# Optimization experiments

Hardware: AMD Instinct MI355X
Metric: run time of the kernel (lower is better)

## Reference

```python
import jax, jax.numpy as jnp
import numpy as np

B, L, DM = 4, 1024, 2048
H, KV, HD = 32, 4, 128
G = H // KV
E, TOPK, MI = 16, 8, 128
EPS = 1e-6
THETA = 1e6


def rms_norm(x, w):
    return x * jax.lax.rsqrt(jnp.mean(x * x, axis=-1, keepdims=True) + EPS) * w


def rotate_half(x):
    x1, x2 = jnp.split(x, 2, axis=-1)
    return jnp.concatenate([-x2, x1], axis=-1)


def setup_inputs() -> dict:
    key = jax.random.key(0)
    ks = jax.random.split(key, 10)
    s = 0.02
    # RoPE tables: [L, HD] broadcast to [B, L, HD]
    inv_freq = 1.0 / (THETA ** (jnp.arange(0, HD, 2, dtype=jnp.float32) / HD))
    ang = jnp.arange(L, dtype=jnp.float32)[:, None] * inv_freq[None, :]
    emb = jnp.concatenate([ang, ang], axis=-1)
    cos = jnp.broadcast_to(jnp.cos(emb)[None], (B, L, HD)).astype(jnp.float32)
    sin = jnp.broadcast_to(jnp.sin(emb)[None], (B, L, HD)).astype(jnp.float32)
    return {
        "x": jax.random.normal(ks[0], (B, L, DM), jnp.float32),
        "cos": cos,
        "sin": sin,
        "norm_attn_w": jnp.ones((DM,), jnp.float32),
        "q_w": jax.random.normal(ks[1], (H * HD, DM), jnp.float32) * s,
        "k_w": jax.random.normal(ks[2], (KV * HD, DM), jnp.float32) * s,
        "v_w": jax.random.normal(ks[3], (KV * HD, DM), jnp.float32) * s,
        "qn_w": jnp.ones((HD,), jnp.float32),
        "kn_w": jnp.ones((HD,), jnp.float32),
        "o_w": jax.random.normal(ks[4], (DM, H * HD), jnp.float32) * s,
        "norm_mlp_w": jnp.ones((DM,), jnp.float32),
        "router_w": jax.random.normal(ks[5], (E, DM), jnp.float32) * s,
        "egw": jax.random.normal(ks[6], (E, MI, DM), jnp.float32) * s,
        "euw": jax.random.normal(ks[7], (E, MI, DM), jnp.float32) * s,
        "edw": jax.random.normal(ks[8], (E, DM, MI), jnp.float32) * s,
    }


def _layer(x, cos, sin, norm_attn_w, q_w, k_w, v_w, qn_w, kn_w, o_w,
           norm_mlp_w, router_w, egw, euw, edw):
    b, l, dm = x.shape
    # ---- attention sub-block ----
    h = rms_norm(x, norm_attn_w)
    q = rms_norm((h @ q_w.T).reshape(b, l, H, HD), qn_w).swapaxes(1, 2)   # [B,H,L,D]
    k = rms_norm((h @ k_w.T).reshape(b, l, KV, HD), kn_w).swapaxes(1, 2)  # [B,KV,L,D]
    v = (h @ v_w.T).reshape(b, l, KV, HD).swapaxes(1, 2)                  # [B,KV,L,D]
    c = cos[:, None]  # [B,1,L,D]
    s = sin[:, None]
    q = c * q + s * rotate_half(q)
    k = c * k + s * rotate_half(k)
    # GQA: repeat kv heads
    k = jnp.repeat(k, G, axis=1)  # [B,H,L,D]
    v = jnp.repeat(v, G, axis=1)
    scores = jnp.einsum("bhqd,bhkd->bhqk", q, k) / jnp.sqrt(jnp.float32(HD))
    causal = jnp.tril(jnp.ones((l, l), bool))
    scores = jnp.where(causal[None, None], scores, jnp.float32(-1e30))
    attn = jax.nn.softmax(scores, axis=-1)
    o = jnp.einsum("bhqk,bhkd->bhqd", attn, v).swapaxes(1, 2).reshape(b, l, H * HD)
    x = x + o @ o_w.T
    # ---- sparse MoE MLP ----
    hm = rms_norm(x, norm_mlp_w).reshape(b * l, dm)  # [N,DM]
    logits = hm @ router_w.T                          # [N,E]
    probs = jax.nn.softmax(logits.astype(jnp.float32), axis=-1)
    rw, sel = jax.lax.top_k(probs, TOPK)              # [N,TOPK]
    rw = (rw / rw.sum(axis=-1, keepdims=True)).astype(x.dtype)
    n = b * l
    # dense combine weights [N,E] (topk indices are unique per token)
    w_dense = jnp.zeros((n, E), x.dtype).at[jnp.arange(n)[:, None], sel].add(rw)

    def body(acc, inp):
        gw, uw, dw, we = inp  # gw/uw [MI,DM], dw [DM,MI], we [N]
        a = jax.nn.silu(hm @ gw.T) * (hm @ uw.T)      # [N,MI]
        return acc + (a @ dw.T) * we[:, None], None

    out, _ = jax.lax.scan(body, jnp.zeros_like(hm), (egw, euw, edw, w_dense.T))
    return x + out.reshape(b, l, dm)


def reference(x, cos, sin, norm_attn_w, q_w, k_w, v_w, qn_w, kn_w, o_w,
              norm_mlp_w, router_w, egw, euw, edw):
    return _layer(x, cos, sin, norm_attn_w, q_w, k_w, v_w, qn_w, kn_w, o_w,
                  norm_mlp_w, router_w, egw, euw, edw)
```

## Files before the change

kernel.cpp:

```cpp
#include <hip/hip_runtime.h>
#include <stdint.h>

typedef _Float16 f16x8 __attribute__((ext_vector_type(8)));
typedef _Float16 f16x4 __attribute__((ext_vector_type(4)));
typedef float    f32x4 __attribute__((ext_vector_type(4)));

__device__ __forceinline__ void load16_lds(const _Float16* g, _Float16* l) {
    __builtin_amdgcn_global_load_lds(
        (const __attribute__((address_space(1))) void*)g,
        (__attribute__((address_space(3))) void*)l, 16, 0, 0);
}


__global__ void k_cast4(const float* __restrict__ q, const float* __restrict__ k,
                        const float* __restrict__ v, const float* __restrict__ o,
                        _Float16* __restrict__ qkvw, _Float16* __restrict__ ow)
{
    size_t i = ((size_t)blockIdx.x * 256 + threadIdx.x) * 4;
    const float* src; _Float16* dst;
    if (i < 8388608)        { src = q + i;            dst = qkvw + i; }
    else if (i < 9437184)   { src = k + (i - 8388608); dst = qkvw + i; }
    else if (i < 10485760)  { src = v + (i - 9437184); dst = qkvw + i; }
    else                    { src = o + (i - 10485760); dst = ow + (i - 10485760); }
    float4 x = *reinterpret_cast<const float4*>(src);
    f16x4 y = { (_Float16)x.x, (_Float16)x.y, (_Float16)x.z, (_Float16)x.w };
    *reinterpret_cast<f16x4*>(dst) = y;
}

__global__ void k_cast_dw(const float* __restrict__ edw, _Float16* __restrict__ dwc) {
    int t = blockIdx.x * 256 + threadIdx.x;
    int mi4 = (t & 31) * 4;
    int dm = (t >> 5) & 2047;
    int e = t >> 16;
    float4 v = *reinterpret_cast<const float4*>(edw + (((size_t)e * 2048 + dm) << 7) + mi4);
    f16x4 o = { (_Float16)v.x, (_Float16)v.y, (_Float16)v.z, (_Float16)v.w };
    *reinterpret_cast<f16x4*>(dwc + ((size_t)dm << 11) + e * 128 + mi4) = o;
}

__global__ __launch_bounds__(256) void k_cast_guw(
    const float* __restrict__ eg, const float* __restrict__ eu,
    _Float16* __restrict__ out)
{
    const int row = blockIdx.x;
    const int e = row >> 8, rem = row & 255, half = rem >> 7, mi = rem & 127;
    const float* src = (half ? eu : eg) + ((size_t)(e * 128 + mi)) * 2048;
    const int c = threadIdx.x * 8;
    float4 v0 = *reinterpret_cast<const float4*>(src + c);
    float4 v1 = *reinterpret_cast<const float4*>(src + c + 4);
    f16x8 o = { (_Float16)v0.x,(_Float16)v0.y,(_Float16)v0.z,(_Float16)v0.w,
                (_Float16)v1.x,(_Float16)v1.y,(_Float16)v1.z,(_Float16)v1.w };
    *reinterpret_cast<f16x8*>(out + (size_t)row * 2048 + c) = o;
}

__global__ void k_ones(_Float16* __restrict__ p) {
    int i = blockIdx.x * 256 + threadIdx.x;
    _Float16 v = (i < 256) ? (_Float16)1.0f : (_Float16)0.0f;
    f16x4 o = { v, v, v, v };
    *reinterpret_cast<f16x4*>(p + i * 4) = o;
}

__global__ __launch_bounds__(256) void k_rmsnorm(
    const float* __restrict__ x, const float* __restrict__ w,
    _Float16* __restrict__ oh)
{
    const int row = blockIdx.x, tid = threadIdx.x;
    const float* xr = x + (size_t)row * 2048;
    float4 a = *reinterpret_cast<const float4*>(xr + tid * 8);
    float4 b = *reinterpret_cast<const float4*>(xr + tid * 8 + 4);
    float ss = a.x*a.x + a.y*a.y + a.z*a.z + a.w*a.w
             + b.x*b.x + b.y*b.y + b.z*b.z + b.w*b.w;
    #pragma unroll
    for (int m = 1; m < 64; m <<= 1) ss += __shfl_xor(ss, m);
    __shared__ float red[4];
    if ((tid & 63) == 0) red[tid >> 6] = ss;
    __syncthreads();
    float tot = red[0] + red[1] + red[2] + red[3];
    float r = rsqrtf(tot * (1.f / 2048.f) + 1e-6f);
    float4 wa = *reinterpret_cast<const float4*>(w + tid * 8);
    float4 wb = *reinterpret_cast<const float4*>(w + tid * 8 + 4);
    f16x8 hv = { (_Float16)(a.x*r*wa.x), (_Float16)(a.y*r*wa.y),
                 (_Float16)(a.z*r*wa.z), (_Float16)(a.w*r*wa.w),
                 (_Float16)(b.x*r*wb.x), (_Float16)(b.y*r*wb.y),
                 (_Float16)(b.z*r*wb.z), (_Float16)(b.w*r*wb.w) };
    *reinterpret_cast<f16x8*>(oh + (size_t)row * 2048 + tid * 8) = hv;
}

__global__ __launch_bounds__(256) void k_gemm(
    const _Float16* __restrict__ A, int lda,
    const _Float16* __restrict__ W, int ldw,
    float* __restrict__ Cf, _Float16* __restrict__ Ch, int ldc,
    const float* __restrict__ resid, int K)
{
    __shared__ __align__(16) _Float16 As[3][128][32];
    __shared__ __align__(16) _Float16 Ws[3][128][32];
    const int r0 = blockIdx.x * 128, c0 = blockIdx.y * 128;
    const int tid = threadIdx.x, lane = tid & 63, wid = tid >> 6;
    const int wr = wid >> 1, wc = wid & 1;
    const int sr = lane >> 2;
    const int scs = ((lane & 3) ^ ((lane >> 3) & 3)) * 8;
    const int fr = lane & 15;
    const int rks = (((lane >> 4) ^ ((fr >> 1) & 3))) * 8;
    const f32x4 z4 = { 0.f, 0.f, 0.f, 0.f };
    f32x4 acc[4][4];
    #pragma unroll
    for (int i = 0; i < 4; i++)
        #pragma unroll
        for (int j = 0; j < 4; j++) acc[i][j] = z4;

    auto stage = [&](int bf, int k0) {
        #pragma unroll
        for (int i = 0; i < 2; i++) {
            int ch = wid * 2 + i;
            load16_lds(A + (size_t)(r0 + ch * 16 + sr) * lda + k0 + scs, &As[bf][ch * 16][0]);
            load16_lds(W + (size_t)(c0 + ch * 16 + sr) * ldw + k0 + scs, &Ws[bf][ch * 16][0]);
        }
    };

    const int nt = K >> 5;
    stage(0, 0);
    if (nt > 1) stage(1, 32);
    int cur = 0;
    for (int t = 0; t < nt; t++) {
        if (t < nt - 1) asm volatile("s_waitcnt vmcnt(4)" ::: "memory");
        else            asm volatile("s_waitcnt vmcnt(0)" ::: "memory");
        __builtin_amdgcn_s_barrier();
        f16x8 af[4], bf4[4];
        #pragma unroll
        for (int i = 0; i < 4; i++)
            af[i] = *reinterpret_cast<const f16x8*>(&As[cur][wr * 64 + i * 16 + fr][rks]);
        #pragma unroll
        for (int j = 0; j < 4; j++)
            bf4[j] = *reinterpret_cast<const f16x8*>(&Ws[cur][wc * 64 + j * 16 + fr][rks]);
        if (t + 2 < nt) stage((t + 2) % 3, (t + 2) << 5);
        __builtin_amdgcn_s_setprio(1);
        #pragma unroll
        for (int i = 0; i < 4; i++)
            #pragma unroll
            for (int j = 0; j < 4; j++)
                acc[i][j] = __builtin_amdgcn_mfma_f32_16x16x32_f16(af[i], bf4[j], acc[i][j], 0, 0, 0);
        __builtin_amdgcn_s_setprio(0);
        cur = (cur + 1) % 3;
    }
    #pragma unroll
    for (int i = 0; i < 4; i++) {
        const int rowb = r0 + wr * 64 + i * 16 + (lane >> 4) * 4;
        #pragma unroll
        for (int j = 0; j < 4; j++) {
            const int col = c0 + wc * 64 + j * 16 + fr;
            #pragma unroll
            for (int r = 0; r < 4; r++) {
                size_t idx = (size_t)(rowb + r) * ldc + col;
                float v = acc[i][j][r];
                if (resid) v += resid[idx];
                if (Ch) Ch[idx] = (_Float16)v;
                else    Cf[idx] = v;
            }
        }
    }
}

__global__ __launch_bounds__(512, 2) void k_gemm8(
    const _Float16* __restrict__ A, int lda,
    const _Float16* __restrict__ W, int ldw,
    _Float16* __restrict__ Ch, int ldc, int K)
{
    __shared__ __align__(16) _Float16 As[3][256][32];
    __shared__ __align__(16) _Float16 Ws[3][256][32];
    const int r0 = blockIdx.x * 256, c0 = blockIdx.y * 256;
    const int tid = threadIdx.x, lane = tid & 63, wid = tid >> 6;
    const int wr = wid >> 2, wc = wid & 3;
    const int rA = lane >> 2;
    const int scs = ((lane & 3) ^ ((lane >> 3) & 3)) * 8;
    const int fr = lane & 15;
    const int rks = (((lane >> 4) ^ ((fr >> 1) & 3))) * 8;
    const f32x4 z4 = { 0.f, 0.f, 0.f, 0.f };
    f32x4 acc[8][4];
    #pragma unroll
    for (int i = 0; i < 8; i++)
        #pragma unroll
        for (int j = 0; j < 4; j++) acc[i][j] = z4;

    auto stage = [&](int bf, int k0) {
        #pragma unroll
        for (int i = 0; i < 2; i++) {
            load16_lds(A + (size_t)(r0 + i * 128 + wid * 16 + rA) * lda + k0 + scs,
                       &As[bf][i * 128 + wid * 16][0]);
            load16_lds(W + (size_t)(c0 + i * 128 + wid * 16 + rA) * ldw + k0 + scs,
                       &Ws[bf][i * 128 + wid * 16][0]);
        }
    };

    const int nt = K >> 5;
    stage(0, 0);
    if (nt > 1) stage(1, 32);
    int cur = 0;
    for (int t = 0; t < nt; t++) {
        if (t < nt - 1) asm volatile("s_waitcnt vmcnt(4)" ::: "memory");
        else            asm volatile("s_waitcnt vmcnt(0)" ::: "memory");
        __builtin_amdgcn_s_barrier();
        f16x8 af[8], bf4[4];
        #pragma unroll
        for (int i = 0; i < 8; i++)
            af[i] = *reinterpret_cast<const f16x8*>(&As[cur][wr * 128 + i * 16 + fr][rks]);
        #pragma unroll
        for (int j = 0; j < 4; j++)
            bf4[j] = *reinterpret_cast<const f16x8*>(&Ws[cur][wc * 64 + j * 16 + fr][rks]);
        if (t + 2 < nt) stage((t + 2) % 3, (t + 2) << 5);
        __builtin_amdgcn_s_setprio(1);
        #pragma unroll
        for (int i = 0; i < 8; i++)
            #pragma unroll
            for (int j = 0; j < 4; j++)
                acc[i][j] = __builtin_amdgcn_mfma_f32_16x16x32_f16(af[i], bf4[j], acc[i][j], 0, 0, 0);
        __builtin_amdgcn_s_setprio(0);
        cur = (cur + 1) % 3;
    }
    #pragma unroll
    for (int i = 0; i < 8; i++) {
        const int rowb = r0 + wr * 128 + i * 16 + (lane >> 4) * 4;
        #pragma unroll
        for (int j = 0; j < 4; j++) {
            const int col = c0 + wc * 64 + j * 16 + fr;
            #pragma unroll
            for (int r = 0; r < 4; r++)
                Ch[(size_t)(rowb + r) * ldc + col] = (_Float16)acc[i][j][r];
        }
    }
}

__global__ __launch_bounds__(256) void k_gu_comb(
    const _Float16* __restrict__ gucat, const float* __restrict__ wdense,
    _Float16* __restrict__ ab)
{
    const int tok = blockIdx.x;
    const int idx = threadIdx.x;
    const int e = idx >> 4, mi8 = (idx & 15) * 8;
    const _Float16* gp = gucat + (size_t)tok * 4096 + e * 256 + mi8;
    f16x8 gv = *reinterpret_cast<const f16x8*>(gp);
    f16x8 uv = *reinterpret_cast<const f16x8*>(gp + 128);
    float wv = wdense[(size_t)e * 4096 + tok];
    f16x8 o;
    #pragma unroll
    for (int j = 0; j < 8; j++) {
        float g = (float)gv[j], u = (float)uv[j];
        float sil = g / (1.f + __expf(-g));
        o[j] = (_Float16)(sil * u * wv);
    }
    *reinterpret_cast<f16x8*>(ab + (size_t)tok * 2048 + e * 128 + mi8) = o;
}

__global__ __launch_bounds__(256) void k_qkv_post(
    const _Float16* __restrict__ qkv,
    const float* __restrict__ cosb, const float* __restrict__ sinb,
    const float* __restrict__ qn_w, const float* __restrict__ kn_w,
    _Float16* __restrict__ qh, _Float16* __restrict__ kh)
{
    const int tok = blockIdx.x;
    const int u = blockIdx.y * 4 + (threadIdx.x >> 6);
    const int lane = threadIdx.x & 63;
    const int b = tok >> 10, l = tok & 1023;
    const float SCL = 0.12752887074166638f;
    const float c0 = cosb[(size_t)tok * 128 + lane];
    const float c1 = cosb[(size_t)tok * 128 + lane + 64];
    const float s0 = sinb[(size_t)tok * 128 + lane];
    const float s1 = sinb[(size_t)tok * 128 + lane + 64];
    if (u < 32) {
        const _Float16* base = qkv + (size_t)tok * 5120 + u * 128;
        float v0 = (float)base[lane], v1 = (float)base[lane + 64];
        float ss = v0 * v0 + v1 * v1;
        #pragma unroll
        for (int m = 1; m < 64; m <<= 1) ss += __shfl_xor(ss, m);
        float rms = rsqrtf(ss * (1.f / 128.f) + 1e-6f);
        float n0 = v0 * rms * qn_w[lane], n1 = v1 * rms * qn_w[lane + 64];
        _Float16* o = qh + (size_t)tok * 4096 + u * 128;
        o[lane]      = (_Float16)(SCL * (c0 * n0 - s0 * n1));
        o[lane + 64] = (_Float16)(SCL * (c1 * n1 + s1 * n0));
    } else {
        const int kvh = u - 32;
        const _Float16* base = qkv + (size_t)tok * 5120 + 4096 + kvh * 128;
        float v0 = (float)base[lane], v1 = (float)base[lane + 64];
        float ss = v0 * v0 + v1 * v1;
        #pragma unroll
        for (int m = 1; m < 64; m <<= 1) ss += __shfl_xor(ss, m);
        float rms = rsqrtf(ss * (1.f / 128.f) + 1e-6f);
        float n0 = v0 * rms * kn_w[lane], n1 = v1 * rms * kn_w[lane + 64];
        _Float16* o = kh + (((size_t)(b * 4 + kvh)) * 1024 + l) * 128;
        o[lane]      = (_Float16)(c0 * n0 - s0 * n1);
        o[lane + 64] = (_Float16)(c1 * n1 + s1 * n0);
    }
}

__global__ __launch_bounds__(256) void k_vt(
    const _Float16* __restrict__ qkv, _Float16* __restrict__ vth)
{
    const int bkv = blockIdx.x;
    const int b = bkv >> 2, kv = bkv & 3;
    const int l0 = blockIdx.y * 64, d0 = blockIdx.z * 64;
    __shared__ _Float16 T[64][72];
    const int t = threadIdx.x;
    const int r = t >> 3, c8 = (t & 7) * 8;
    #pragma unroll
    for (int rr = 0; rr < 2; rr++) {
        int l = l0 + r + rr * 32;
        *reinterpret_cast<f16x8*>(&T[r + rr * 32][c8]) =
            *reinterpret_cast<const f16x8*>(
                qkv + (size_t)(b * 1024 + l) * 5120 + 4608 + kv * 128 + d0 + c8);
    }
    __syncthreads();
    #pragma unroll
    for (int rr = 0; rr < 2; rr++) {
        int d = d0 + r + rr * 32;
        f16x8 v;
        #pragma unroll
        for (int j = 0; j < 8; j++) v[j] = T[c8 + j][r + rr * 32];
        *reinterpret_cast<f16x8*>(vth + ((size_t)(bkv * 128 + d)) * 1024 + l0 + c8) = v;
    }
}

__global__ __launch_bounds__(256) void k_attn(
    const _Float16* __restrict__ qh, const _Float16* __restrict__ kh,
    const _Float16* __restrict__ vth, const _Float16* __restrict__ ones16,
    _Float16* __restrict__ oh)
{
    const int bh = blockIdx.x;
    const int g = 15 - blockIdx.y;
    const int b = bh >> 5, h = bh & 31, kv = h >> 3;
    const int tid = threadIdx.x, lane = tid & 63, wid = tid >> 6;
    const int fr = lane & 15, fg = lane >> 4;
    const int q0w = g * 64 + wid * 16;

    __shared__ __align__(16) _Float16 Ks[64][128];
    __shared__ __align__(16) _Float16 Vs[144][64];
    __shared__ __align__(16) _Float16 Ps[4][16][72];

    const _Float16* kb = kh + ((size_t)(b * 4 + kv)) * 1024 * 128;
    const _Float16* vb = vth + ((size_t)(b * 4 + kv)) * 128 * 1024;

    f16x8 aq[4];
    {
        const _Float16* qbase = qh + ((size_t)(b * 1024 + q0w + fr)) * 4096 + h * 128;
        #pragma unroll
        for (int kk = 0; kk < 4; kk++)
            aq[kk] = *reinterpret_cast<const f16x8*>(qbase + kk * 32 + fg * 8);
    }

    float m_r[4] = { -1e30f, -1e30f, -1e30f, -1e30f };
    const f32x4 z4 = { 0.f, 0.f, 0.f, 0.f };
    f32x4 oacc[9];
    #pragma unroll
    for (int dj = 0; dj < 9; dj++) oacc[dj] = z4;

    const int ntiles = g + 1;
    for (int kt = 0; kt < ntiles; kt++) {
        const int key0 = kt * 64;
        #pragma unroll
        for (int i = 0; i < 4; i++) {
            int rr = 16 * wid + 4 * i + (lane >> 4);
            int c16 = (lane & 15) ^ (rr & 15);
            load16_lds(kb + (size_t)(key0 + rr) * 128 + c16 * 8,
                       &Ks[0][0] + (16 * wid + 4 * i) * 128);
        }
        #pragma unroll
        for (int i = 0; i < 4; i++) {
            int rr = 32 * wid + 8 * i + (lane >> 3);
            int c16 = (lane & 7) ^ (rr & 7);
            load16_lds(vb + (size_t)rr * 1024 + key0 + c16 * 8,
                       &Vs[0][0] + (32 * wid + 8 * i) * 64);
        }
        if (wid < 2) {
            int rr = wid * 8 + (lane >> 3);
            int c16 = (lane & 7) ^ (rr & 7);
            load16_lds(ones16 + (size_t)rr * 1024 + key0 + c16 * 8,
                       &Vs[0][0] + (128 + wid * 8) * 64);
        }
        __syncthreads();

        f32x4 sc[4];
        #pragma unroll
        for (int j = 0; j < 4; j++) sc[j] = z4;
        #pragma unroll
        for (int j = 0; j < 4; j++) {
            #pragma unroll
            for (int kk = 0; kk < 4; kk++) {
                f16x8 bk = *reinterpret_cast<const f16x8*>(
                    &Ks[0][0] + (j * 16 + fr) * 128 + (((kk * 4 + fg) ^ fr) * 8));
                sc[j] = __builtin_amdgcn_mfma_f32_16x16x32_f16(aq[kk], bk, sc[j], 0, 0, 0);
            }
        }

        const bool lastt = (kt == ntiles - 1);
        float pmax[4] = { -1e30f, -1e30f, -1e30f, -1e30f };
        #pragma unroll
        for (int j = 0; j < 4; j++) {
            const int key = key0 + j * 16 + fr;
            #pragma unroll
            for (int r = 0; r < 4; r++) {
                float v = sc[j][r];
                if (lastt && key > q0w + fg * 4 + r) v = -1e30f;
                sc[j][r] = v;
                pmax[r] = fmaxf(pmax[r], v);
            }
        }
        #pragma unroll
        for (int m = 1; m < 16; m <<= 1)
            #pragma unroll
            for (int r = 0; r < 4; r++) pmax[r] = fmaxf(pmax[r], __shfl_xor(pmax[r], m));

        float dm = fmaxf(fmaxf(pmax[0] - m_r[0], pmax[1] - m_r[1]),
                         fmaxf(pmax[2] - m_r[2], pmax[3] - m_r[3]));
        if (__any(dm > 8.f)) {
            #pragma unroll
            for (int r = 0; r < 4; r++) {
                float mn = fmaxf(m_r[r], pmax[r]);
                float alpha = __builtin_amdgcn_exp2f(m_r[r] - mn);
                m_r[r] = mn;
                #pragma unroll
                for (int dj = 0; dj < 9; dj++) oacc[dj][r] *= alpha;
            }
        }
        #pragma unroll
        for (int j = 0; j < 4; j++)
            #pragma unroll
            for (int r = 0; r < 4; r++)
                sc[j][r] = __builtin_amdgcn_exp2f(sc[j][r] - m_r[r]);

        #pragma unroll
        for (int j = 0; j < 4; j++)
            #pragma unroll
            for (int r = 0; r < 4; r++)
                Ps[wid][fg * 4 + r][j * 16 + fr] = (_Float16)sc[j][r];

        #pragma unroll
        for (int ks = 0; ks < 2; ks++) {
            f16x8 ap = *reinterpret_cast<const f16x8*>(&Ps[wid][fr][ks * 32 + fg * 8]);
            #pragma unroll
            for (int dj = 0; dj < 9; dj++) {
                f16x8 bv = *reinterpret_cast<const f16x8*>(
                    &Vs[0][0] + (dj * 16 + fr) * 64 + (((ks * 4 + fg) ^ (fr & 7)) * 8));
                oacc[dj] = __builtin_amdgcn_mfma_f32_16x16x32_f16(ap, bv, oacc[dj], 0, 0, 0);
            }
        }
        __syncthreads();
    }

    float inv[4];
    #pragma unroll
    for (int r = 0; r < 4; r++) {
        float l = __shfl(oacc[8][r], lane & 48);
        inv[r] = 1.f / l;
    }
    #pragma unroll
    for (int dj = 0; dj < 8; dj++)
        #pragma unroll
        for (int r = 0; r < 4; r++)
            oh[((size_t)(b * 1024 + q0w + fg * 4 + r)) * 4096 + h * 128 + dj * 16 + fr] =
                (_Float16)(oacc[dj][r] * inv[r]);
}

__global__ __launch_bounds__(256) void k_router(
    const float* __restrict__ x2, const float* __restrict__ wm,
    const float* __restrict__ rw, float* __restrict__ wdense)
{
    const int tok = blockIdx.x * 4 + (threadIdx.x >> 6);
    const int lane = threadIdx.x & 63;
    __shared__ float lg[4][16];
    const float* hr = x2 + (size_t)tok * 2048;
    float vals[32];
    float ss = 0.f;
    #pragma unroll
    for (int i = 0; i < 32; i++) { float v = hr[i * 64 + lane]; vals[i] = v; ss += v * v; }
    #pragma unroll
    for (int m = 1; m < 64; m <<= 1) ss += __shfl_xor(ss, m);
    float r = rsqrtf(ss * (1.f / 2048.f) + 1e-6f);
    #pragma unroll
    for (int i = 0; i < 32; i++) vals[i] *= r * wm[i * 64 + lane];
    for (int e = 0; e < 16; e++) {
        float acc = 0.f;
        #pragma unroll
        for (int i = 0; i < 32; i++) acc += vals[i] * rw[(size_t)e * 2048 + i * 64 + lane];
        #pragma unroll
        for (int m = 1; m < 64; m <<= 1) acc += __shfl_xor(acc, m);
        if (lane == 0) lg[threadIdx.x >> 6][e] = acc;
    }
    __syncthreads();
    if (lane == 0) {
        float* l = lg[threadIdx.x >> 6];
        float mx = l[0];
        for (int e = 1; e < 16; e++) mx = fmaxf(mx, l[e]);
        float p[16]; float sum = 0.f;
        for (int e = 0; e < 16; e++) { p[e] = expf(l[e] - mx); sum += p[e]; }
        for (int e = 0; e < 16; e++) p[e] /= sum;
        bool sel[16]; for (int e = 0; e < 16; e++) sel[e] = false;
        float ssum = 0.f;
        for (int t = 0; t < 8; t++) {
            int bi = -1; float bv = -1.f;
            for (int e = 0; e < 16; e++) if (!sel[e] && p[e] > bv) { bv = p[e]; bi = e; }
            sel[bi] = true; ssum += bv;
        }
        for (int e = 0; e < 16; e++)
            wdense[(size_t)e * 4096 + tok] = sel[e] ? p[e] / ssum : 0.f;
    }
}


extern "C" void kernel_launch(void* const* d_in, const int* in_sizes, int n_in,
                              void* d_out, int out_size, void* d_ws, size_t ws_size,
                              hipStream_t stream)
{
    const float* x        = (const float*)d_in[0];
    const float* cosb     = (const float*)d_in[1];
    const float* sinb     = (const float*)d_in[2];
    const float* nattn    = (const float*)d_in[3];
    const float* q_w      = (const float*)d_in[4];
    const float* k_w      = (const float*)d_in[5];
    const float* v_w      = (const float*)d_in[6];
    const float* qn_w     = (const float*)d_in[7];
    const float* kn_w     = (const float*)d_in[8];
    const float* o_w      = (const float*)d_in[9];
    const float* nmlp     = (const float*)d_in[10];
    const float* router_w = (const float*)d_in[11];
    const float* egw      = (const float*)d_in[12];
    const float* euw      = (const float*)d_in[13];
    const float* edw      = (const float*)d_in[14];

    char* w = (char*)d_ws;
    _Float16* qkvw_h = (_Float16*)(w + 0);
    _Float16* ow_h   = (_Float16*)(w + 20971520);
    _Float16* guw_h  = (_Float16*)(w + 37748736);
    _Float16* dwc_h  = (_Float16*)(w + 54525952);
    _Float16* h_h    = (_Float16*)(w + 62914560);
    _Float16* hm_h   = h_h;
    float*    x2     = (float*)(w + 79691776);
    _Float16* qkv_h  = (_Float16*)(w + 113246208);
    _Float16* o_h    = qkv_h;
    _Float16* ab_h   = qkv_h;
    _Float16* q_h    = (_Float16*)(w + 155189248);
    _Float16* gucat  = (_Float16*)(w + 155189248);
    _Float16* k_h    = (_Float16*)(w + 188743680);
    _Float16* vt_h   = (_Float16*)(w + 192937984);
    float*    wdense = (float*)(w + 197132288);
    _Float16* ones_h = (_Float16*)(w + 197394432);

    k_cast4<<<18432, 256, 0, stream>>>(q_w, k_w, v_w, o_w, qkvw_h, ow_h);
    k_cast_guw<<<4096, 256, 0, stream>>>(egw, euw, guw_h);
    k_cast_dw<<<4096, 256, 0, stream>>>(edw, dwc_h);
    k_ones<<<16, 256, 0, stream>>>(ones_h);

    k_rmsnorm<<<4096, 256, 0, stream>>>(x, nattn, h_h);
    k_gemm8<<<dim3(16, 16), 512, 0, stream>>>(h_h, 2048, qkvw_h, 2048, qkv_h, 5120, 2048);
    k_gemm<<<dim3(32, 8), 256, 0, stream>>>(h_h, 2048, qkvw_h + (size_t)4096 * 2048, 2048,
                                            nullptr, qkv_h + 4096, 5120, nullptr, 2048);
    k_qkv_post<<<dim3(4096, 9), 256, 0, stream>>>(qkv_h, cosb, sinb, qn_w, kn_w, q_h, k_h);
    k_vt<<<dim3(16, 16, 2), 256, 0, stream>>>(qkv_h, vt_h);
    k_attn<<<dim3(128, 16), 256, 0, stream>>>(q_h, k_h, vt_h, ones_h, o_h);
    k_gemm<<<dim3(32, 16), 256, 0, stream>>>(o_h, 4096, ow_h, 4096,
                                             x2, nullptr, 2048, x, 4096);
    k_rmsnorm<<<4096, 256, 0, stream>>>(x2, nmlp, hm_h);
    k_router<<<1024, 256, 0, stream>>>(x2, nmlp, router_w, wdense);
    k_gemm8<<<dim3(16, 16), 512, 0, stream>>>(hm_h, 2048, guw_h, 2048, gucat, 4096, 2048);
    k_gu_comb<<<4096, 256, 0, stream>>>(gucat, wdense, ab_h);
    k_gemm<<<dim3(32, 16), 256, 0, stream>>>(ab_h, 2048, dwc_h, 2048,
                                             (float*)d_out, nullptr, 2048, x2, 2048);

    (void)in_sizes; (void)n_in; (void)out_size; (void)ws_size;
}
```

Measured before the change: 512.6 us.

## Fuse SwiGLU combine into gate/up GEMM epilogue and double-buffer attention K/V

The MoE gate/up GEMM now applies SiLU(gate)*up and the routing weight in its epilogue, staging results through the reused LDS buffers. This removes the separate combine kernel and the write and re-read of the intermediate gate/up tensor. Separately, the attention kernel double-buffers K/V tiles in LDS and prefetches the next tile while computing the current one. Its ones-row for the softmax denominator moves to a small persistent LDS buffer loaded once, replacing per-tile reloads and a trailing barrier, at the cost of more LDS and extra epilogue barriers in the GEMM.

```diff
diff --git a/kernel.cpp b/kernel.cpp
--- a/kernel.cpp
+++ b/kernel.cpp
@@ -54,7 +54,7 @@
 
 __global__ void k_ones(_Float16* __restrict__ p) {
     int i = blockIdx.x * 256 + threadIdx.x;
-    _Float16 v = (i < 256) ? (_Float16)1.0f : (_Float16)0.0f;
+    _Float16 v = (i < 16) ? (_Float16)1.0f : (_Float16)0.0f;
     f16x4 o = { v, v, v, v };
     *reinterpret_cast<f16x4*>(p + i * 4) = o;
 }
@@ -162,7 +162,8 @@
 __global__ __launch_bounds__(512, 2) void k_gemm8(
     const _Float16* __restrict__ A, int lda,
     const _Float16* __restrict__ W, int ldw,
-    _Float16* __restrict__ Ch, int ldc, int K)
+    _Float16* __restrict__ Ch, int ldc, int K,
+    const float* __restrict__ wdense, _Float16* __restrict__ ab)
 {
     __shared__ __align__(16) _Float16 As[3][256][32];
     __shared__ __align__(16) _Float16 Ws[3][256][32];
@@ -171,7 +172,7 @@
     const int wr = wid >> 2, wc = wid & 3;
     const int rA = lane >> 2;
     const int scs = ((lane & 3) ^ ((lane >> 3) & 3)) * 8;
-    const int fr = lane & 15;
+    const int fr = lane & 15, fg = lane >> 4;
     const int rks = (((lane >> 4) ^ ((fr >> 1) & 3))) * 8;
     const f32x4 z4 = { 0.f, 0.f, 0.f, 0.f };
     f32x4 acc[8][4];
@@ -215,38 +216,72 @@
         __builtin_amdgcn_s_setprio(0);
         cur = (cur + 1) % 3;
     }
-    #pragma unroll
-    for (int i = 0; i < 8; i++) {
-        const int rowb = r0 + wr * 128 + i * 16 + (lane >> 4) * 4;
-        #pragma unroll
-        for (int j = 0; j < 4; j++) {
-            const int col = c0 + wc * 64 + j * 16 + fr;
-            #pragma unroll
-            for (int r = 0; r < 4; r++)
-                Ch[(size_t)(rowb + r) * ldc + col] = (_Float16)acc[i][j][r];
-        }
-    }
-}
-
-__global__ __launch_bounds__(256) void k_gu_comb(
-    const _Float16* __restrict__ gucat, const float* __restrict__ wdense,
-    _Float16* __restrict__ ab)
-{
-    const int tok = blockIdx.x;
-    const int idx = threadIdx.x;
-    const int e = idx >> 4, mi8 = (idx & 15) * 8;
-    const _Float16* gp = gucat + (size_t)tok * 4096 + e * 256 + mi8;
-    f16x8 gv = *reinterpret_cast<const f16x8*>(gp);
-    f16x8 uv = *reinterpret_cast<const f16x8*>(gp + 128);
-    float wv = wdense[(size_t)e * 4096 + tok];
-    f16x8 o;
-    #pragma unroll
-    for (int j = 0; j < 8; j++) {
-        float g = (float)gv[j], u = (float)uv[j];
-        float sil = g / (1.f + __expf(-g));
-        o[j] = (_Float16)(sil * u * wv);
-    }
-    *reinterpret_cast<f16x8*>(ab + (size_t)tok * 2048 + e * 128 + mi8) = o;
+
+    if (!wdense) {
+        #pragma unroll
+        for (int i = 0; i < 8; i++) {
+            const int rowb = r0 + wr * 128 + i * 16 + fg * 4;
+            #pragma unroll
+            for (int j = 0; j < 4; j++) {
+                const int col = c0 + wc * 64 + j * 16 + fr;
+                #pragma unroll
+                for (int r = 0; r < 4; r++)
+                    Ch[(size_t)(rowb + r) * ldc + col] = (_Float16)acc[i][j][r];
+            }
+        }
+        return;
+    }
+
+    _Float16* LgA = &As[0][0][0];
+    _Float16* LgB = &Ws[0][0][0];
+    auto lgp = [&](int row, int mi) -> _Float16* {
+        return ((row < 128) ? LgA : LgB) + (size_t)(row & 127) * 136 + mi;
+    };
+    const int e = blockIdx.y;
+    __syncthreads();
+    if (wc < 2) {
+        #pragma unroll
+        for (int i = 0; i < 8; i++) {
+            const int row = wr * 128 + i * 16 + fg * 4;
+            #pragma unroll
+            for (int j = 0; j < 4; j++) {
+                const int mi = wc * 64 + j * 16 + fr;
+                #pragma unroll
+                for (int r = 0; r < 4; r++)
+                    *lgp(row + r, mi) = (_Float16)acc[i][j][r];
+            }
+        }
+    }
+    __syncthreads();
+    if (wc >= 2) {
+        #pragma unroll
+        for (int i = 0; i < 8; i++) {
+            const int row = wr * 128 + i * 16 + fg * 4;
+            #pragma unroll
+            for (int j = 0; j < 4; j++) {
+                const int mi = (wc - 2) * 64 + j * 16 + fr;
+                #pragma unroll
+                for (int r = 0; r < 4; r++) {
+                    float g = (float)*lgp(row + r, mi);
+                    float sil = g / (1.f + __expf(-g));
+                    *lgp(row + r, mi) = (_Float16)(sil * acc[i][j][r]);
+                }
+            }
+        }
+    }
+    __syncthreads();
+    #pragma unroll
+    for (int pass = 0; pass < 8; pass++) {
+        int cid = pass * 512 + tid;
+        int row = cid >> 4, col8 = cid & 15;
+        f16x8 v = *reinterpret_cast<const f16x8*>(
+            ((row < 128) ? LgA : LgB) + (size_t)(row & 127) * 136 + col8 * 8);
+        float wv = wdense[(size_t)e * 4096 + r0 + row];
+        f16x8 o;
+        #pragma unroll
+        for (int j = 0; j < 8; j++) o[j] = (_Float16)((float)v[j] * wv);
+        *reinterpret_cast<f16x8*>(ab + (size_t)(r0 + row) * 2048 + e * 128 + col8 * 8) = o;
+    }
 }
 
 __global__ __launch_bounds__(256) void k_qkv_post(
@@ -329,51 +364,58 @@
     const int fr = lane & 15, fg = lane >> 4;
     const int q0w = g * 64 + wid * 16;
 
-    __shared__ __align__(16) _Float16 Ks[64][128];
-    __shared__ __align__(16) _Float16 Vs[144][64];
+    __shared__ __align__(16) _Float16 Ks[2][64][128];
+    __shared__ __align__(16) _Float16 Vs[2][128][64];
+    __shared__ __align__(16) _Float16 Vones[16][64];
     __shared__ __align__(16) _Float16 Ps[4][16][72];
 
     const _Float16* kb = kh + ((size_t)(b * 4 + kv)) * 1024 * 128;
     const _Float16* vb = vth + ((size_t)(b * 4 + kv)) * 128 * 1024;
 
-    f16x8 aq[4];
-    {
-        const _Float16* qbase = qh + ((size_t)(b * 1024 + q0w + fr)) * 4096 + h * 128;
-        #pragma unroll
-        for (int kk = 0; kk < 4; kk++)
-            aq[kk] = *reinterpret_cast<const f16x8*>(qbase + kk * 32 + fg * 8);
-    }
-
-    float m_r[4] = { -1e30f, -1e30f, -1e30f, -1e30f };
-    const f32x4 z4 = { 0.f, 0.f, 0.f, 0.f };
-    f32x4 oacc[9];
-    #pragma unroll
-    for (int dj = 0; dj < 9; dj++) oacc[dj] = z4;
-
-    const int ntiles = g + 1;
-    for (int kt = 0; kt < ntiles; kt++) {
-        const int key0 = kt * 64;
+    auto stage = [&](int nb, int key0) {
         #pragma unroll
         for (int i = 0; i < 4; i++) {
             int rr = 16 * wid + 4 * i + (lane >> 4);
             int c16 = (lane & 15) ^ (rr & 15);
             load16_lds(kb + (size_t)(key0 + rr) * 128 + c16 * 8,
-                       &Ks[0][0] + (16 * wid + 4 * i) * 128);
+                       &Ks[nb][0][0] + (16 * wid + 4 * i) * 128);
         }
         #pragma unroll
         for (int i = 0; i < 4; i++) {
             int rr = 32 * wid + 8 * i + (lane >> 3);
             int c16 = (lane & 7) ^ (rr & 7);
             load16_lds(vb + (size_t)rr * 1024 + key0 + c16 * 8,
-                       &Vs[0][0] + (32 * wid + 8 * i) * 64);
-        }
-        if (wid < 2) {
-            int rr = wid * 8 + (lane >> 3);
-            int c16 = (lane & 7) ^ (rr & 7);
-            load16_lds(ones16 + (size_t)rr * 1024 + key0 + c16 * 8,
-                       &Vs[0][0] + (128 + wid * 8) * 64);
-        }
-        __syncthreads();
+                       &Vs[nb][0][0] + (32 * wid + 8 * i) * 64);
+        }
+    };
+
+    f16x8 aq[4];
+    {
+        const _Float16* qbase = qh + ((size_t)(b * 1024 + q0w + fr)) * 4096 + h * 128;
+        #pragma unroll
+        for (int kk = 0; kk < 4; kk++)
+            aq[kk] = *reinterpret_cast<const f16x8*>(qbase + kk * 32 + fg * 8);
+    }
+    if (wid == 0) {
+        #pragma unroll
+        for (int i = 0; i < 2; i++)
+            load16_lds(ones16 + (size_t)(lane + i * 64) * 8, &Vones[0][0] + i * 512);
+    }
+    stage(0, 0);
+
+    float m_r[4] = { -1e30f, -1e30f, -1e30f, -1e30f };
+    const f32x4 z4 = { 0.f, 0.f, 0.f, 0.f };
+    f32x4 oacc[9];
+    #pragma unroll
+    for (int dj = 0; dj < 9; dj++) oacc[dj] = z4;
+
+    const int ntiles = g + 1;
+    int cb = 0;
+    for (int kt = 0; kt < ntiles; kt++) {
+        const int key0 = kt * 64;
+        asm volatile("s_waitcnt vmcnt(0)" ::: "memory");
+        __builtin_amdgcn_s_barrier();
+        if (kt + 1 < ntiles) stage(cb ^ 1, key0 + 64);
 
         f32x4 sc[4];
         #pragma unroll
@@ -383,7 +425,7 @@
             #pragma unroll
             for (int kk = 0; kk < 4; kk++) {
                 f16x8 bk = *reinterpret_cast<const f16x8*>(
-                    &Ks[0][0] + (j * 16 + fr) * 128 + (((kk * 4 + fg) ^ fr) * 8));
+                    &Ks[cb][0][0] + (j * 16 + fr) * 128 + (((kk * 4 + fg) ^ fr) * 8));
                 sc[j] = __builtin_amdgcn_mfma_f32_16x16x32_f16(aq[kk], bk, sc[j], 0, 0, 0);
             }
         }
@@ -434,13 +476,16 @@
         for (int ks = 0; ks < 2; ks++) {
             f16x8 ap = *reinterpret_cast<const f16x8*>(&Ps[wid][fr][ks * 32 + fg * 8]);
             #pragma unroll
-            for (int dj = 0; dj < 9; dj++) {
+            for (int dj = 0; dj < 8; dj++) {
                 f16x8 bv = *reinterpret_cast<const f16x8*>(
-                    &Vs[0][0] + (dj * 16 + fr) * 64 + (((ks * 4 + fg) ^ (fr & 7)) * 8));
+                    &Vs[cb][0][0] + (dj * 16 + fr) * 64 + (((ks * 4 + fg) ^ (fr & 7)) * 8));
                 oacc[dj] = __builtin_amdgcn_mfma_f32_16x16x32_f16(ap, bv, oacc[dj], 0, 0, 0);
             }
-        }
-        __syncthreads();
+            f16x8 bo = *reinterpret_cast<const f16x8*>(
+                &Vones[0][0] + fr * 64 + (((ks * 4 + fg) ^ (fr & 7)) * 8));
+            oacc[8] = __builtin_amdgcn_mfma_f32_16x16x32_f16(ap, bo, oacc[8], 0, 0, 0);
+        }
+        cb ^= 1;
     }
 
     float inv[4];
@@ -535,7 +580,6 @@
     _Float16* o_h    = qkv_h;
     _Float16* ab_h   = qkv_h;
     _Float16* q_h    = (_Float16*)(w + 155189248);
-    _Float16* gucat  = (_Float16*)(w + 155189248);
     _Float16* k_h    = (_Float16*)(w + 188743680);
     _Float16* vt_h   = (_Float16*)(w + 192937984);
     float*    wdense = (float*)(w + 197132288);
@@ -544,10 +588,11 @@
     k_cast4<<<18432, 256, 0, stream>>>(q_w, k_w, v_w, o_w, qkvw_h, ow_h);
     k_cast_guw<<<4096, 256, 0, stream>>>(egw, euw, guw_h);
     k_cast_dw<<<4096, 256, 0, stream>>>(edw, dwc_h);
-    k_ones<<<16, 256, 0, stream>>>(ones_h);
+    k_ones<<<1, 256, 0, stream>>>(ones_h);
 
     k_rmsnorm<<<4096, 256, 0, stream>>>(x, nattn, h_h);
-    k_gemm8<<<dim3(16, 16), 512, 0, stream>>>(h_h, 2048, qkvw_h, 2048, qkv_h, 5120, 2048);
+    k_gemm8<<<dim3(16, 16), 512, 0, stream>>>(h_h, 2048, qkvw_h, 2048, qkv_h, 5120, 2048,
+                                              nullptr, nullptr);
     k_gemm<<<dim3(32, 8), 256, 0, stream>>>(h_h, 2048, qkvw_h + (size_t)4096 * 2048, 2048,
                                             nullptr, qkv_h + 4096, 5120, nullptr, 2048);
     k_qkv_post<<<dim3(4096, 9), 256, 0, stream>>>(qkv_h, cosb, sinb, qn_w, kn_w, q_h, k_h);
@@ -557,8 +602,8 @@
                                              x2, nullptr, 2048, x, 4096);
     k_rmsnorm<<<4096, 256, 0, stream>>>(x2, nmlp, hm_h);
     k_router<<<1024, 256, 0, stream>>>(x2, nmlp, router_w, wdense);
-    k_gemm8<<<dim3(16, 16), 512, 0, stream>>>(hm_h, 2048, guw_h, 2048, gucat, 4096, 2048);
-    k_gu_comb<<<4096, 256, 0, stream>>>(gucat, wdense, ab_h);
+    k_gemm8<<<dim3(16, 16), 512, 0, stream>>>(hm_h, 2048, guw_h, 2048, nullptr, 0, 2048,
+                                              wdense, ab_h);
     k_gemm<<<dim3(32, 16), 256, 0, stream>>>(ab_h, 2048, dwc_h, 2048,
                                              (float*)d_out, nullptr, 2048, x2, 2048);
 
```

Measured after the change: 504.7 us. No clear change (-1.5%).
